# Kernel optimization log

Measured on AMD Instinct MI355X. Metric: run time of the kernel, lower is better.

Reference implementation:

```python
import jax, jax.numpy as jnp
import numpy as np

BATCH, NSTEPS, IN_F, OUT_F = 8192, 16, 256, 512


def setup_inputs() -> dict:
    key = jax.random.key(0)
    ks = jax.random.split(key, 20)
    r = jax.random.normal
    return {
        "x": r(ks[0], (BATCH, NSTEPS, IN_F), jnp.float32),
        "C": r(ks[1], (BATCH, OUT_F, 1), jnp.float32),
        "H": r(ks[2], (BATCH, OUT_F, 1), jnp.float32),
        "fg_w_c": r(ks[3], (OUT_F, 1), jnp.float32),
        "fg_w_h": r(ks[4], (OUT_F, OUT_F), jnp.float32),
        "fg_w_x": r(ks[5], (OUT_F, IN_F), jnp.float32),
        "fg_b": r(ks[6], (OUT_F, 1), jnp.float32),
        "ig_w_c": r(ks[7], (OUT_F, 1), jnp.float32),
        "ig_w_h": r(ks[8], (OUT_F, OUT_F), jnp.float32),
        "ig_w_x": r(ks[9], (OUT_F, IN_F), jnp.float32),
        "ig_b": r(ks[10], (OUT_F, 1), jnp.float32),
        "in_w_h": r(ks[11], (OUT_F, OUT_F), jnp.float32),
        "in_w_x": r(ks[12], (OUT_F, IN_F), jnp.float32),
        "in_b": r(ks[13], (OUT_F, 1), jnp.float32),
        "og_w_cn": r(ks[14], (OUT_F, 1), jnp.float32),
        "og_w_h": r(ks[15], (OUT_F, OUT_F), jnp.float32),
        "og_w_x": r(ks[16], (OUT_F, IN_F), jnp.float32),
        "og_b": r(ks[17], (OUT_F, 1), jnp.float32),
        "n": 3,
    }


def reference(x, C, H,
              fg_w_c, fg_w_h, fg_w_x, fg_b,
              ig_w_c, ig_w_h, ig_w_x, ig_b,
              in_w_h, in_w_x, in_b,
              og_w_cn, og_w_h, og_w_x, og_b,
              n):
    # x: [B, T, IN] -> current step [B, IN, 1]
    x_cur = x[:, n, :, None]
    # peephole LSTM gates; matmul broadcasts [O,O] @ [B,O,1] -> [B,O,1]
    fg = jax.nn.sigmoid(fg_w_c * C + jnp.matmul(fg_w_h, H) + jnp.matmul(fg_w_x, x_cur) + fg_b)
    ig = jax.nn.sigmoid(ig_w_c * C + jnp.matmul(ig_w_h, H) + jnp.matmul(ig_w_x, x_cur) + ig_b)
    inn = jnp.tanh(jnp.matmul(in_w_h, H) + jnp.matmul(in_w_x, x_cur) + in_b)
    cm = fg * C + ig * inn
    og = jax.nn.sigmoid(og_w_cn * cm + jnp.matmul(og_w_h, H) + jnp.matmul(og_w_x, x_cur) + og_b)
    h = og * jnp.tanh(cm)
    return (cm, h)
```

## Files before the change

### kernel.cpp

```cpp
#include <hip/hip_runtime.h>


typedef _Float16 half8 __attribute__((ext_vector_type(8)));
typedef _Float16 half4v __attribute__((ext_vector_type(4)));
typedef float floatx4 __attribute__((ext_vector_type(4)));

#define BATCH 8192
#define NSTEPS 16
#define IN_F 256
#define OUT_F 512
#define KDIM 768
#define NDIM 2048
#define HSIZE ((size_t)BATCH * OUT_F)

#define BM 256
#define BN 256
#define BK 64
#define NKT (KDIM / BK)

__device__ __forceinline__ void async_copy16(const void* gptr, void* lptr) {
  __builtin_amdgcn_global_load_lds(
      (const __attribute__((address_space(1))) unsigned int*)gptr,
      (__attribute__((address_space(3))) unsigned int*)lptr,
      16, 0, 0);
}

__device__ __forceinline__ float sigmoidf_(float x) {
  return 1.0f / (1.0f + __expf(-x));
}

__device__ __forceinline__ float tanhf_(float x) {
  x = fminf(fmaxf(x, -20.0f), 20.0f);
  float e = __expf(2.0f * x);
  return (e - 1.0f) / (e + 1.0f);
}

#define PACK_ROWS 8
__global__ void pack_AW(const float* __restrict__ H, const float* __restrict__ x,
                        const int* __restrict__ nptr,
                        const float* __restrict__ fg_w_h, const float* __restrict__ fg_w_x,
                        const float* __restrict__ ig_w_h, const float* __restrict__ ig_w_x,
                        const float* __restrict__ in_w_h, const float* __restrict__ in_w_x,
                        const float* __restrict__ og_w_h, const float* __restrict__ og_w_x,
                        _Float16* __restrict__ A, _Float16* __restrict__ W) {
  const int k = threadIdx.x * 4;
  const int n = *nptr;
  const int row0 = blockIdx.x * PACK_ROWS;
#pragma unroll
  for (int rr = 0; rr < PACK_ROWS; ++rr) {
    const int blk = row0 + rr;
    const float* src;
    _Float16* dst;
    if (blk < BATCH) {
      const int b = blk;
      if (k < OUT_F) {
        src = H + (size_t)b * OUT_F + k;
      } else {
        src = x + ((size_t)b * NSTEPS + n) * IN_F + (k - OUT_F);
      }
      dst = A + (size_t)b * KDIM + k;
    } else {
      const int row = blk - BATCH;
      const int g  = (row >> 4) & 3;
      const int jj = ((row >> 6) << 4) | (row & 15);
      if (k < OUT_F) {
        const float* wh = (g == 0) ? fg_w_h : (g == 1) ? ig_w_h : (g == 2) ? in_w_h : og_w_h;
        src = wh + (size_t)jj * OUT_F + k;
      } else {
        const float* wx = (g == 0) ? fg_w_x : (g == 1) ? ig_w_x : (g == 2) ? in_w_x : og_w_x;
        src = wx + (size_t)jj * IN_F + (k - OUT_F);
      }
      dst = W + (size_t)row * KDIM + k;
    }
    float4 v = *(const float4*)src;
    half4v h = {(_Float16)v.x, (_Float16)v.y, (_Float16)v.z, (_Float16)v.w};
    *(half4v*)dst = h;
  }
}

__global__ __launch_bounds__(512, 2) void gemm_lstm(
    const _Float16* __restrict__ A, const _Float16* __restrict__ W,
    const float* __restrict__ C,
    const float* __restrict__ fg_w_c, const float* __restrict__ fg_b,
    const float* __restrict__ ig_w_c, const float* __restrict__ ig_b,
    const float* __restrict__ in_b,
    const float* __restrict__ og_w_cn, const float* __restrict__ og_b,
    float* __restrict__ out) {
  __shared__ __align__(16) char smem[131072];

  const int tid = threadIdx.x;
  const int lane = tid & 63;
  const int wave = tid >> 6;
  const int quad = lane >> 4;
  const int l16 = lane & 15;
  const int wm = wave >> 2;
  const int wn = wave & 3;
  const int m0 = blockIdx.y * BM;
  const int n0 = blockIdx.x * BN;

  const int jj = (((n0 + wn * 64) >> 6) << 4) | l16;
  const float fwc = fg_w_c[jj], fb = fg_b[jj];
  const float iwc = ig_w_c[jj], ib = ig_b[jj];
  const float nb  = in_b[jj];
  const float owc = og_w_cn[jj], ob = og_b[jj];

  floatx4 acc[8][4] = {};

  auto stage = [&](int p, int kt) {
    _Float16* As = (_Float16*)(smem + p * 65536);
    _Float16* Bs = (_Float16*)(smem + p * 65536 + 32768);
#pragma unroll
    for (int r = 0; r < 4; ++r) {
      const int g = r * 512 + tid;
      const int row = g >> 3;
      const int cl = g & 7;
      const int cg = cl ^ (row & 7);
      async_copy16(A + (size_t)(m0 + row) * KDIM + kt + cg * 8, As + g * 8);
      async_copy16(W + (size_t)(n0 + row) * KDIM + kt + cg * 8, Bs + g * 8);
    }
  };

  stage(0, 0);
  __syncthreads();

  int cur = 0;
  for (int t = 0; t < NKT; ++t) {
    if (t + 1 < NKT) stage(cur ^ 1, (t + 1) * BK);
    const _Float16* As = (const _Float16*)(smem + cur * 65536);
    const _Float16* Bs = (const _Float16*)(smem + cur * 65536 + 32768);
#pragma unroll
    for (int ks = 0; ks < 2; ++ks) {
      half8 af[8], bf[4];
#pragma unroll
      for (int j = 0; j < 4; ++j) {
        const int row = wn * 64 + j * 16 + l16;
        const int chunk = ks * 4 + quad;
        const int gran = row * 8 + (chunk ^ (row & 7));
        bf[j] = *(const half8*)(Bs + gran * 8);
      }
#pragma unroll
      for (int i = 0; i < 8; ++i) {
        const int row = wm * 128 + i * 16 + l16;
        const int chunk = ks * 4 + quad;
        const int gran = row * 8 + (chunk ^ (row & 7));
        af[i] = *(const half8*)(As + gran * 8);
      }
#pragma unroll
      for (int i = 0; i < 8; ++i)
#pragma unroll
        for (int j = 0; j < 4; ++j)
          acc[i][j] = __builtin_amdgcn_mfma_f32_16x16x32_f16(af[i], bf[j], acc[i][j], 0, 0, 0);
    }
    __syncthreads();
    cur ^= 1;
  }

  float* cmS = (float*)smem;
  float* hS  = (float*)(smem + 65536);

  const int jjloc = wn * 16 + l16;
#pragma unroll
  for (int i = 0; i < 8; ++i) {
    const int rbase = m0 + wm * 128 + i * 16 + quad * 4;
    float cv[4];
#pragma unroll
    for (int r = 0; r < 4; ++r)
      cv[r] = C[(size_t)(rbase + r) * OUT_F + jj];
#pragma unroll
    for (int r = 0; r < 4; ++r) {
      const float c = cv[r];
      const float inn = tanhf_(acc[i][2][r] + nb);
      const float fg  = sigmoidf_(fwc * c + acc[i][0][r] + fb);
      const float ig  = sigmoidf_(iwc * c + acc[i][1][r] + ib);
      const float cm  = fg * c + ig * inn;
      const float og  = sigmoidf_(owc * cm + acc[i][3][r] + ob);
      const int rloc = wm * 128 + i * 16 + quad * 4 + r;
      cmS[rloc * 64 + jjloc] = cm;
      hS [rloc * 64 + jjloc] = og * tanhf_(cm);
    }
  }
  __syncthreads();

  const int ub = blockIdx.x * 64;
#pragma unroll
  for (int q = 0; q < 8; ++q) {
    const int idx = q * 512 + tid;
    const int row = idx >> 4;
    const int c4 = idx & 15;
    const size_t gbase = (size_t)(m0 + row) * OUT_F + ub + c4 * 4;
    *(float4*)(out + gbase) = *(const float4*)(cmS + row * 64 + c4 * 4);
    *(float4*)(out + HSIZE + gbase) = *(const float4*)(hS + row * 64 + c4 * 4);
  }
}

extern "C" void kernel_launch(void* const* d_in, const int* in_sizes, int n_in,
                              void* d_out, int out_size, void* d_ws, size_t ws_size,
                              hipStream_t stream) {
  const float* x       = (const float*)d_in[0];
  const float* C       = (const float*)d_in[1];
  const float* H       = (const float*)d_in[2];
  const float* fg_w_c  = (const float*)d_in[3];
  const float* fg_w_h  = (const float*)d_in[4];
  const float* fg_w_x  = (const float*)d_in[5];
  const float* fg_b    = (const float*)d_in[6];
  const float* ig_w_c  = (const float*)d_in[7];
  const float* ig_w_h  = (const float*)d_in[8];
  const float* ig_w_x  = (const float*)d_in[9];
  const float* ig_b    = (const float*)d_in[10];
  const float* in_w_h  = (const float*)d_in[11];
  const float* in_w_x  = (const float*)d_in[12];
  const float* in_b    = (const float*)d_in[13];
  const float* og_w_cn = (const float*)d_in[14];
  const float* og_w_h  = (const float*)d_in[15];
  const float* og_w_x  = (const float*)d_in[16];
  const float* og_b    = (const float*)d_in[17];
  const int*   nptr    = (const int*)d_in[18];

  char* ws = (char*)d_ws;
  _Float16* Apk = (_Float16*)ws;
  _Float16* Wpk = (_Float16*)(ws + 12582912);
  (void)ws_size; (void)in_sizes; (void)n_in; (void)out_size;

  pack_AW<<<(BATCH + NDIM) / PACK_ROWS, 192, 0, stream>>>(
      H, x, nptr,
      fg_w_h, fg_w_x, ig_w_h, ig_w_x,
      in_w_h, in_w_x, og_w_h, og_w_x,
      Apk, Wpk);
  dim3 grid(NDIM / BN, BATCH / BM);
  gemm_lstm<<<grid, 512, 0, stream>>>(Apk, Wpk, C,
                                      fg_w_c, fg_b, ig_w_c, ig_b, in_b,
                                      og_w_cn, og_b, (float*)d_out);
}
```

Before: 258.9 us.

## Pipeline GEMM main loop with partial vmcnt waits, split barriers and XCD block swizzle

Replaces the 2D grid with a 1D grid whose block index is swizzled so that consecutive blocks, which are dispatched round-robin across the 8 XCDs, map to related tiles and share L2 reuse. The main loop now waits only for the previous stage's async loads (vmcnt(8)) and uses raw s_barrier instead of __syncthreads. Each k-slice is split into two halves with a barrier and s_setprio around the MFMA bursts, so that waves interleave LDS reads and matrix work. The hand-written waitcnt and barriers risk subtle races and add extra barriers per iteration.

New measurement: 261.2 us. No clear change (+0.9%).

```diff
diff --git a/kernel.cpp b/kernel.cpp
--- a/kernel.cpp
+++ b/kernel.cpp
@@ -95,8 +95,13 @@
   const int l16 = lane & 15;
   const int wm = wave >> 2;
   const int wn = wave & 3;
-  const int m0 = blockIdx.y * BM;
-  const int n0 = blockIdx.x * BN;
+
+  const int bid = blockIdx.x;
+  const int swz = (bid & 7) * 32 + (bid >> 3);
+  const int bx = swz & 7;
+  const int by = swz >> 3;
+  const int m0 = by * BM;
+  const int n0 = bx * BN;
 
   const int jj = (((n0 + wn * 64) >> 6) << 4) | l16;
   const float fwc = fg_w_c[jj], fb = fg_b[jj];
@@ -106,9 +111,10 @@
 
   floatx4 acc[8][4] = {};
 
-  auto stage = [&](int p, int kt) {
+  auto stage = [&](int p, int t) {
     _Float16* As = (_Float16*)(smem + p * 65536);
     _Float16* Bs = (_Float16*)(smem + p * 65536 + 32768);
+    const int kt = t * BK;
 #pragma unroll
     for (int r = 0; r < 4; ++r) {
       const int g = r * 512 + tid;
@@ -121,38 +127,53 @@
   };
 
   stage(0, 0);
-  __syncthreads();
-
-  int cur = 0;
+
   for (int t = 0; t < NKT; ++t) {
-    if (t + 1 < NKT) stage(cur ^ 1, (t + 1) * BK);
-    const _Float16* As = (const _Float16*)(smem + cur * 65536);
-    const _Float16* Bs = (const _Float16*)(smem + cur * 65536 + 32768);
+    if (t + 1 < NKT) {
+      stage((t + 1) & 1, t + 1);
+      asm volatile("s_waitcnt vmcnt(8)" ::: "memory");
+    } else {
+      asm volatile("s_waitcnt vmcnt(0)" ::: "memory");
+    }
+    asm volatile("s_barrier" ::: "memory");
+
+    const _Float16* As = (const _Float16*)(smem + (t & 1) * 65536);
+    const _Float16* Bs = (const _Float16*)(smem + (t & 1) * 65536 + 32768);
+
+    half8 bf[4];
 #pragma unroll
     for (int ks = 0; ks < 2; ++ks) {
-      half8 af[8], bf[4];
-#pragma unroll
-      for (int j = 0; j < 4; ++j) {
-        const int row = wn * 64 + j * 16 + l16;
-        const int chunk = ks * 4 + quad;
-        const int gran = row * 8 + (chunk ^ (row & 7));
-        bf[j] = *(const half8*)(Bs + gran * 8);
+#pragma unroll
+      for (int ih = 0; ih < 2; ++ih) {
+        if (ih == 0) {
+#pragma unroll
+          for (int j = 0; j < 4; ++j) {
+            const int row = wn * 64 + j * 16 + l16;
+            const int chunk = ks * 4 + quad;
+            const int gran = row * 8 + (chunk ^ (row & 7));
+            bf[j] = *(const half8*)(Bs + gran * 8);
+          }
+        }
+        half8 af[4];
+#pragma unroll
+        for (int i = 0; i < 4; ++i) {
+          const int row = wm * 128 + (ih * 4 + i) * 16 + l16;
+          const int chunk = ks * 4 + quad;
+          const int gran = row * 8 + (chunk ^ (row & 7));
+          af[i] = *(const half8*)(As + gran * 8);
+        }
+        asm volatile("s_barrier" ::: "memory");
+        __builtin_amdgcn_s_setprio(1);
+#pragma unroll
+        for (int i = 0; i < 4; ++i)
+#pragma unroll
+          for (int j = 0; j < 4; ++j)
+            acc[ih * 4 + i][j] = __builtin_amdgcn_mfma_f32_16x16x32_f16(
+                af[i], bf[j], acc[ih * 4 + i][j], 0, 0, 0);
+        __builtin_amdgcn_s_setprio(0);
       }
-#pragma unroll
-      for (int i = 0; i < 8; ++i) {
-        const int row = wm * 128 + i * 16 + l16;
-        const int chunk = ks * 4 + quad;
-        const int gran = row * 8 + (chunk ^ (row & 7));
-        af[i] = *(const half8*)(As + gran * 8);
-      }
-#pragma unroll
-      for (int i = 0; i < 8; ++i)
-#pragma unroll
-        for (int j = 0; j < 4; ++j)
-          acc[i][j] = __builtin_amdgcn_mfma_f32_16x16x32_f16(af[i], bf[j], acc[i][j], 0, 0, 0);
-    }
-    __syncthreads();
-    cur ^= 1;
+    }
+    asm volatile("s_barrier" ::: "memory");
   }
 
   float* cmS = (float*)smem;
@@ -181,7 +202,7 @@
   }
   __syncthreads();
 
-  const int ub = blockIdx.x * 64;
+  const int ub = bx * 64;
 #pragma unroll
   for (int q = 0; q < 8; ++q) {
     const int idx = q * 512 + tid;
@@ -226,8 +247,7 @@
       fg_w_h, fg_w_x, ig_w_h, ig_w_x,
       in_w_h, in_w_x, og_w_h, og_w_x,
       Apk, Wpk);
-  dim3 grid(NDIM / BN, BATCH / BM);
-  gemm_lstm<<<grid, 512, 0, stream>>>(Apk, Wpk, C,
-                                      fg_w_c, fg_b, ig_w_c, ig_b, in_b,
-                                      og_w_cn, og_b, (float*)d_out);
-}
+  gemm_lstm<<<dim3(256), 512, 0, stream>>>(Apk, Wpk, C,
+                                           fg_w_c, fg_b, ig_w_c, ig_b, in_b,
+                                           og_w_cn, og_b, (float*)d_out);
+}
```
